# Performance work log

Measured on AMD Instinct MI355X. Metric: run time of the kernel, lower is better.

Reference implementation:

```python
import jax, jax.numpy as jnp
import numpy as np

NEG_INF = -1000000000.0
B, S, E, H = 2, 2048, 1024, 16
HD = E // H


def setup_inputs() -> dict:
    key = jax.random.key(0)
    ks = jax.random.split(key, 5)
    sd = 1.0 / np.sqrt(E)
    return {
        "x": jax.random.normal(ks[0], (B, S, E), dtype=jnp.float32),
        "Wqkv": jax.random.normal(ks[1], (3 * E, E), dtype=jnp.float32) * sd,
        "bqkv": jax.random.normal(ks[2], (3 * E,), dtype=jnp.float32) * sd,
        "Wout": jax.random.normal(ks[3], (E, E), dtype=jnp.float32) * sd,
        "bout": jax.random.normal(ks[4], (E,), dtype=jnp.float32) * sd,
    }


def reference(x, Wqkv, bqkv, Wout, bout):
    # qkv projection (torch Linear: x @ W.T + b)
    qkv = x @ Wqkv.T + bqkv                      # [B, S, 3E]
    qkv = qkv.reshape(B, S, H, 3 * HD).transpose(0, 2, 1, 3)  # [B, H, S, 3*hd]
    q, k, v = jnp.split(qkv, 3, axis=-1)          # each [B, H, S, hd]
    scaled = jnp.einsum('bhqd,bhkd->bhqk', q, k) / jnp.sqrt(jnp.float32(HD))
    # faithful to source: mask = tril(ones) * NEG_INF (lower triangle incl. diagonal gets -1e9)
    mask = jnp.tril(jnp.ones((S, S), dtype=jnp.float32)) * NEG_INF
    scaled = scaled + mask                        # broadcast over [B, H]
    attention = jax.nn.softmax(scaled, axis=-1)
    values = jnp.einsum('bhqk,bhkd->bhqd', attention, v)
    values = values.transpose(0, 2, 1, 3).reshape(B, S, E)
    out = values @ Wout.T + bout
    return out
```

## Files before the change

kernel.cpp:

```cpp
#include <hip/hip_runtime.h>
#include <hip/hip_bf16.h>
#include <math.h>

#define Bb 2
#define Ss 2048
#define Ee 1024
#define Hh 16
#define HDd 64
#define NEG_INF_F -1000000000.0f

typedef __attribute__((ext_vector_type(8))) short bfrag;
typedef __attribute__((ext_vector_type(4))) float ffrag;
typedef __attribute__((ext_vector_type(16))) float ffrag16;
typedef __attribute__((ext_vector_type(8))) unsigned short us8;

#define C1F 0.1803368801f

__device__ __forceinline__ unsigned short f2bf(float x) {
  unsigned u = __float_as_uint(x);
  u += 0x7fffu + ((u >> 16) & 1u);
  return (unsigned short)(u >> 16);
}
__device__ __forceinline__ float bf2f(unsigned short h) {
  return __uint_as_float(((unsigned)h) << 16);
}

__device__ __forceinline__ void async_copy16(void* lds, const void* g) {
  __builtin_amdgcn_global_load_lds(
      (const __attribute__((address_space(1))) unsigned int*)g,
      (__attribute__((address_space(3))) unsigned int*)lds, 16, 0, 0);
}

__global__ __launch_bounds__(256) void split_all(
    const float* __restrict__ x, unsigned short* __restrict__ xh,
    const float* __restrict__ wq, unsigned short* __restrict__ wqh,
    unsigned short* __restrict__ wql,
    const float* __restrict__ wo, unsigned short* __restrict__ woh,
    unsigned short* __restrict__ wol) {
  int bid = blockIdx.x;
  const float* in;
  unsigned short *hi, *lo;
  if (bid < 4096) { in = x; hi = xh; lo = nullptr; }
  else if (bid < 7168) { bid -= 4096; in = wq; hi = wqh; lo = wql; }
  else { bid -= 7168; in = wo; hi = woh; lo = wol; }
  const int idx = (bid * 256 + threadIdx.x) * 4;
  const float4 v = *(const float4*)(in + idx);
  unsigned short h0 = f2bf(v.x), h1 = f2bf(v.y), h2 = f2bf(v.z), h3 = f2bf(v.w);
  ushort4 hv = {h0, h1, h2, h3};
  *(ushort4*)(hi + idx) = hv;
  if (lo) {
    ushort4 lv = {f2bf(v.x - bf2f(h0)), f2bf(v.y - bf2f(h1)),
                  f2bf(v.z - bf2f(h2)), f2bf(v.w - bf2f(h3))};
    *(ushort4*)(lo + idx) = lv;
  }
}

__device__ __forceinline__ int gemm_slot(int row, int q) {
  return (row >> 1) * 8 + ((((row & 1) * 4) | q) ^ ((row >> 1) & 7));
}
__device__ __forceinline__ int slot_src_off(int slot, int ld) {
  const int dr = slot >> 3;
  const int idx8 = (slot & 7) ^ (dr & 7);
  const int row = dr * 2 + (idx8 >> 2);
  const int q = idx8 & 3;
  return row * ld + q * 8;
}

__global__ __launch_bounds__(256) void gemm_qkv(
    const unsigned short* __restrict__ Ah,
    const unsigned short* __restrict__ Bh, const unsigned short* __restrict__ Bl,
    const float* __restrict__ bias,
    unsigned short* __restrict__ q_h,
    unsigned short* __restrict__ k_h, unsigned short* __restrict__ k_l,
    unsigned short* __restrict__ vt_h) {
  __shared__ unsigned short sm[3 * 4096];
  const int tid = threadIdx.x;
  const int lane = tid & 63;
  const int w = tid >> 6;
  const int wm = w >> 1;
  const int wn = w & 1;
  const int l31 = lane & 31;
  const int e = lane >> 5;
  const int m0 = blockIdx.x * 128;
  const int n0 = blockIdx.y * 128;

  int coff[2], ldsb[2];
#pragma unroll
  for (int u = 0; u < 2; ++u) {
    const int slot = w * 128 + u * 64 + lane;
    coff[u] = slot_src_off(slot, 1024);
    ldsb[u] = (w * 128 + u * 64) * 8;
  }
  const unsigned short* srcs[3] = {
      Ah + (size_t)m0 * 1024, Bh + (size_t)n0 * 1024, Bl + (size_t)n0 * 1024};

  ffrag16 acc[2][2];
#pragma unroll
  for (int i = 0; i < 2; ++i)
#pragma unroll
    for (int j = 0; j < 2; ++j) acc[i][j] = (ffrag16)0.f;

  int ca[2][2], cb[2][2];
#pragma unroll
  for (int t = 0; t < 2; ++t)
#pragma unroll
    for (int h2 = 0; h2 < 2; ++h2) {
      ca[t][h2] = gemm_slot(wm * 64 + t * 32 + l31, h2 * 2 + e) * 8;
      cb[t][h2] = gemm_slot(wn * 64 + t * 32 + l31, h2 * 2 + e) * 8;
    }

  for (int k0 = 0; k0 < 1024; k0 += 32) {
    __syncthreads();
#pragma unroll
    for (int t = 0; t < 3; ++t)
#pragma unroll
      for (int u = 0; u < 2; ++u)
        async_copy16(&sm[t * 4096 + ldsb[u]], srcs[t] + coff[u] + k0);
    __syncthreads();

    bfrag ah[2][2], bhf[2][2], blf[2][2];
#pragma unroll
    for (int t = 0; t < 2; ++t)
#pragma unroll
      for (int h2 = 0; h2 < 2; ++h2) {
        ah[t][h2] = *(const bfrag*)&sm[0 * 4096 + ca[t][h2]];
        bhf[t][h2] = *(const bfrag*)&sm[1 * 4096 + cb[t][h2]];
        blf[t][h2] = *(const bfrag*)&sm[2 * 4096 + cb[t][h2]];
      }
#pragma unroll
    for (int mt = 0; mt < 2; ++mt)
#pragma unroll
      for (int nt = 0; nt < 2; ++nt)
#pragma unroll
        for (int h2 = 0; h2 < 2; ++h2) {
          acc[mt][nt] = __builtin_amdgcn_mfma_f32_32x32x16_bf16(
              ah[mt][h2], bhf[nt][h2], acc[mt][nt], 0, 0, 0);
          acc[mt][nt] = __builtin_amdgcn_mfma_f32_32x32x16_bf16(
              ah[mt][h2], blf[nt][h2], acc[mt][nt], 0, 0, 0);
        }
  }

#pragma unroll
  for (int nt = 0; nt < 2; ++nt) {
    const int n = n0 + wn * 64 + nt * 32 + l31;
    const float bv = bias[n];
    const int h = n / 192;
    const int c = n - h * 192;
    const int d = c & 63;
#pragma unroll
    for (int mt = 0; mt < 2; ++mt) {
      if (c >= 128) {
#pragma unroll
        for (int g = 0; g < 4; ++g) {
          const int m = m0 + wm * 64 + mt * 32 + g * 8 + e * 4;
          const int bidx = m >> 11;
          const int s = m & 2047;
          ushort4 hv4;
          unsigned short* ph = (unsigned short*)&hv4;
#pragma unroll
          for (int r = 0; r < 4; ++r)
            ph[r] = f2bf(acc[mt][nt][g * 4 + r] + bv);
          const size_t off =
              (size_t)(bidx * 16 + h) * (64 * 2048) + (size_t)d * 2048 + s;
          *(ushort4*)(vt_h + off) = hv4;
        }
      } else if (c < 64) {
#pragma unroll
        for (int g = 0; g < 4; ++g)
#pragma unroll
          for (int r = 0; r < 4; ++r) {
            const int m = m0 + wm * 64 + mt * 32 + g * 8 + e * 4 + r;
            const int bidx = m >> 11;
            const int s = m & 2047;
            const size_t off =
                (size_t)(bidx * 16 + h) * (2048 * 64) + (size_t)s * 64 + d;
            q_h[off] = f2bf((acc[mt][nt][g * 4 + r] + bv) * C1F);
          }
      } else {
#pragma unroll
        for (int g = 0; g < 4; ++g)
#pragma unroll
          for (int r = 0; r < 4; ++r) {
            const int m = m0 + wm * 64 + mt * 32 + g * 8 + e * 4 + r;
            const int bidx = m >> 11;
            const int s = m & 2047;
            const float val = acc[mt][nt][g * 4 + r] + bv;
            const unsigned short hv = f2bf(val);
            const size_t off =
                (size_t)(bidx * 16 + h) * (2048 * 64) + (size_t)s * 64 + d;
            k_h[off] = hv;
            k_l[off] = f2bf(val - bf2f(hv));
          }
      }
    }
  }
}

__global__ __launch_bounds__(256) void gemm_out2(
    const unsigned short* __restrict__ A,
    const unsigned short* __restrict__ Bh, const unsigned short* __restrict__ Bl,
    const float* __restrict__ bias, float* __restrict__ out) {
  __shared__ unsigned short sm[8192];
  const int tid = threadIdx.x;
  const int lane = tid & 63;
  const int w = tid >> 6;
  const int wm = w >> 1;
  const int wn = w & 1;
  const int l31 = lane & 31;
  const int e = lane >> 5;
  const int m0 = blockIdx.x * 128;
  const int n0 = blockIdx.y * 64;

  int acoff[2], aldsb[2];
#pragma unroll
  for (int u = 0; u < 2; ++u) {
    const int slot = w * 128 + u * 64 + lane;
    acoff[u] = slot_src_off(slot, 1024);
    aldsb[u] = (w * 128 + u * 64) * 8;
  }
  const int bslot = w * 64 + lane;
  const int bcoff = slot_src_off(bslot, 1024);
  const int bldsb = bslot * 8;

  const unsigned short* Ap  = A + (size_t)m0 * 1024;
  const unsigned short* Bph = Bh + (size_t)n0 * 1024;
  const unsigned short* Bpl = Bl + (size_t)n0 * 1024;

  ffrag16 acc[2];
  acc[0] = (ffrag16)0.f;
  acc[1] = (ffrag16)0.f;

  int ca[2][2], cb[2];
#pragma unroll
  for (int t = 0; t < 2; ++t)
#pragma unroll
    for (int h2 = 0; h2 < 2; ++h2)
      ca[t][h2] = gemm_slot(wm * 64 + t * 32 + l31, h2 * 2 + e) * 8;
#pragma unroll
  for (int h2 = 0; h2 < 2; ++h2)
    cb[h2] = gemm_slot(wn * 32 + l31, h2 * 2 + e) * 8;

  for (int k0 = 0; k0 < 1024; k0 += 32) {
    __syncthreads();
#pragma unroll
    for (int u = 0; u < 2; ++u)
      async_copy16(&sm[0 + aldsb[u]], Ap + acoff[u] + k0);
    async_copy16(&sm[4096 + bldsb], Bph + bcoff + k0);
    async_copy16(&sm[6144 + bldsb], Bpl + bcoff + k0);
    __syncthreads();

    bfrag ah[2][2], bhf[2], blf[2];
#pragma unroll
    for (int t = 0; t < 2; ++t)
#pragma unroll
      for (int h2 = 0; h2 < 2; ++h2)
        ah[t][h2] = *(const bfrag*)&sm[0 + ca[t][h2]];
#pragma unroll
    for (int h2 = 0; h2 < 2; ++h2) {
      bhf[h2] = *(const bfrag*)&sm[4096 + cb[h2]];
      blf[h2] = *(const bfrag*)&sm[6144 + cb[h2]];
    }
#pragma unroll
    for (int mt = 0; mt < 2; ++mt)
#pragma unroll
      for (int h2 = 0; h2 < 2; ++h2) {
        acc[mt] = __builtin_amdgcn_mfma_f32_32x32x16_bf16(
            ah[mt][h2], bhf[h2], acc[mt], 0, 0, 0);
        acc[mt] = __builtin_amdgcn_mfma_f32_32x32x16_bf16(
            ah[mt][h2], blf[h2], acc[mt], 0, 0, 0);
      }
  }

  const int n = n0 + wn * 32 + l31;
  const float bv = bias[n];
#pragma unroll
  for (int mt = 0; mt < 2; ++mt)
#pragma unroll
    for (int g = 0; g < 4; ++g)
#pragma unroll
      for (int r = 0; r < 4; ++r) {
        const int m = m0 + wm * 64 + mt * 32 + g * 8 + e * 4 + r;
        out[(size_t)m * 1024 + n] = acc[mt][g * 4 + r] + bv;
      }
}

__global__ __launch_bounds__(256) void attn_pair(
    const unsigned short* __restrict__ qh,
    const unsigned short* __restrict__ kh, const unsigned short* __restrict__ kl,
    const unsigned short* __restrict__ vth,
    unsigned short* __restrict__ vals) {
  __shared__ unsigned short sm[2 * 12288 + 8192];
  const int tid = threadIdx.x;
  const int lane = tid & 63;
  const int w = tid >> 6;
  const int l15 = lane & 15;
  const int quad = lane >> 4;
  const int bh = blockIdx.x;
  const int y = blockIdx.y;
  const int rbase[2] = {64 * y + 16 * w, 64 * (31 - y) + 16 * w};
  const int ktB = 31 - y;
  const bool fix = (y == 0) && (w == 3);
  const size_t base = (size_t)bh * (Ss * HDd);
  const int PB = 24576;

  bfrag Qh[2][2];
#pragma unroll
  for (int mt = 0; mt < 2; ++mt)
#pragma unroll
    for (int ks = 0; ks < 2; ++ks) {
      const size_t off = base + (size_t)(rbase[mt] + l15) * 64 + ks * 32 + quad * 8;
      Qh[mt][ks] = *(const bfrag*)(qh + off);
    }

  bfrag vone;
#pragma unroll
  for (int j = 0; j < 8; ++j) vone[j] = (short)0x3F80;

  const int c0 = w * 128 + lane;
  const int c1 = c0 + 64;
  const int r0 = c0 >> 3, r1 = c1 >> 3;
  const int s0 = ((c0 & 7) ^ (r0 & 7)) * 8;
  const int s1 = ((c1 & 7) ^ (r1 & 7)) * 8;
  const int koff0 = r0 * 64 + s0, koff1 = r1 * 64 + s1;
  const int voff0 = r0 * 2048 + s0, voff1 = r1 * 2048 + s1;
  const int ldsc0 = (w * 128) * 8;
  const int ldsc1 = (w * 128 + 64) * 8;

  ffrag O[2][4], Oe[2], Vsum[4];
#pragma unroll
  for (int mt = 0; mt < 2; ++mt) {
#pragma unroll
    for (int dt = 0; dt < 4; ++dt) O[mt][dt] = (ffrag)0.f;
    Oe[mt] = (ffrag)0.f;
  }
#pragma unroll
  for (int dt = 0; dt < 4; ++dt) Vsum[dt] = (ffrag)0.f;

  {
    const unsigned short* kph = kh + base + y * 4096;
    const unsigned short* kpl = kl + base + y * 4096;
    const unsigned short* vph = vth + base + y * 64;
    async_copy16(&sm[0 + ldsc0], kph + koff0);
    async_copy16(&sm[0 + ldsc1], kph + koff1);
    async_copy16(&sm[4096 + ldsc0], kpl + koff0);
    async_copy16(&sm[4096 + ldsc1], kpl + koff1);
    async_copy16(&sm[8192 + ldsc0], vph + voff0);
    async_copy16(&sm[8192 + ldsc1], vph + voff1);
  }

  int bufo = 0;
  for (int kt = y; kt < 32; ++kt) {
    __syncthreads();
    if (kt + 1 < 32) {
      const int alt = bufo ^ 12288;
      const unsigned short* kph = kh + base + (kt + 1) * 4096;
      const unsigned short* kpl = kl + base + (kt + 1) * 4096;
      const unsigned short* vph = vth + base + (kt + 1) * 64;
      async_copy16(&sm[alt + 0 + ldsc0], kph + koff0);
      async_copy16(&sm[alt + 0 + ldsc1], kph + koff1);
      async_copy16(&sm[alt + 4096 + ldsc0], kpl + koff0);
      async_copy16(&sm[alt + 4096 + ldsc1], kpl + koff1);
      async_copy16(&sm[alt + 8192 + ldsc0], vph + voff0);
      async_copy16(&sm[alt + 8192 + ldsc1], vph + voff1);
    }
    const bool bact = (kt >= ktB);

    ffrag S[2][4];
#pragma unroll
    for (int mt = 0; mt < 2; ++mt)
#pragma unroll
      for (int nt = 0; nt < 4; ++nt) S[mt][nt] = (ffrag)0.f;
#pragma unroll
    for (int nt = 0; nt < 4; ++nt) {
      const int krow = nt * 16 + l15;
#pragma unroll
      for (int ks = 0; ks < 2; ++ks) {
        const int koffr = bufo + krow * 64 + ((ks * 4 + quad) ^ (krow & 7)) * 8;
        const bfrag kbh = *(const bfrag*)&sm[koffr];
        const bfrag kbl = *(const bfrag*)&sm[4096 + koffr];
        S[0][nt] = __builtin_amdgcn_mfma_f32_16x16x32_bf16(Qh[0][ks], kbh, S[0][nt], 0, 0, 0);
        S[0][nt] = __builtin_amdgcn_mfma_f32_16x16x32_bf16(Qh[0][ks], kbl, S[0][nt], 0, 0, 0);
        if (bact) {
          S[1][nt] = __builtin_amdgcn_mfma_f32_16x16x32_bf16(Qh[1][ks], kbh, S[1][nt], 0, 0, 0);
          S[1][nt] = __builtin_amdgcn_mfma_f32_16x16x32_bf16(Qh[1][ks], kbl, S[1][nt], 0, 0, 0);
        }
      }
    }

    const float CM = -1.442695041e9f;
#pragma unroll
    for (int mt = 0; mt < 2; ++mt) {
      if (mt == 1 && !bact) continue;
      const bool partial = (kt == (mt == 0 ? y : ktB));
#pragma unroll
      for (int nt = 0; nt < 4; ++nt) {
        const int key = nt * 16 + l15;
#pragma unroll
        for (int rp = 0; rp < 2; ++rp) {
          float t0 = S[mt][nt][2 * rp];
          float t1 = S[mt][nt][2 * rp + 1];
          if (partial) {
            const int jg = kt * 64 + key;
            const int ig = rbase[mt] + quad * 4 + 2 * rp;
            if (jg <= ig) t0 += CM;
            if (jg <= ig + 1) t1 += CM;
          }
          float2 pf;
          pf.x = __builtin_amdgcn_exp2f(t0);
          pf.y = __builtin_amdgcn_exp2f(t1);
          const __hip_bfloat162 pb = __float22bfloat162_rn(pf);
          const unsigned short* pbs = (const unsigned short*)&pb;
          const int prow0 = w * 32 + mt * 16 + quad * 4 + 2 * rp;
          sm[PB + prow0 * 64 + (((key >> 3) ^ (prow0 & 7)) * 8 + (key & 7))] = pbs[0];
          const int prow1 = prow0 + 1;
          sm[PB + prow1 * 64 + (((key >> 3) ^ (prow1 & 7)) * 8 + (key & 7))] = pbs[1];
        }
      }
    }

#pragma unroll
    for (int ks = 0; ks < 2; ++ks) {
      bfrag pA[2];
#pragma unroll
      for (int mt = 0; mt < 2; ++mt) {
        if (mt == 1 && !bact) continue;
        const int prow = w * 32 + mt * 16 + l15;
        pA[mt] = *(const bfrag*)&sm[PB + prow * 64 + ((ks * 4 + quad) ^ (prow & 7)) * 8];
      }
      Oe[0] = __builtin_amdgcn_mfma_f32_16x16x32_bf16(pA[0], vone, Oe[0], 0, 0, 0);
      if (bact)
        Oe[1] = __builtin_amdgcn_mfma_f32_16x16x32_bf16(pA[1], vone, Oe[1], 0, 0, 0);
#pragma unroll
      for (int dt = 0; dt < 4; ++dt) {
        const int vrow = dt * 16 + l15;
        const int voffr = bufo + 8192 + vrow * 64 + ((ks * 4 + quad) ^ (vrow & 7)) * 8;
        const bfrag vbh = *(const bfrag*)&sm[voffr];
        O[0][dt] = __builtin_amdgcn_mfma_f32_16x16x32_bf16(pA[0], vbh, O[0][dt], 0, 0, 0);
        if (bact)
          O[1][dt] = __builtin_amdgcn_mfma_f32_16x16x32_bf16(pA[1], vbh, O[1][dt], 0, 0, 0);
        if (fix)
          Vsum[dt] = __builtin_amdgcn_mfma_f32_16x16x32_bf16(vone, vbh, Vsum[dt], 0, 0, 0);
      }
    }
    bufo ^= 12288;
  }

  const int b = bh >> 4;
  const int h = bh & 15;
#pragma unroll
  for (int mt = 0; mt < 2; ++mt)
#pragma unroll
    for (int r = 0; r < 4; ++r) {
      const float inv = 1.0f / Oe[mt][r];
      const int s = rbase[mt] + quad * 4 + r;
      const size_t rowoff = ((size_t)b * 2048 + s) * 1024 + h * 64;
#pragma unroll
      for (int dt = 0; dt < 4; ++dt) {
        float val = O[mt][dt][r] * inv;
        if (fix && mt == 1 && quad == 3 && r == 3)
          val = Vsum[dt][r] * (1.0f / 2048.0f);
        vals[rowoff + dt * 16 + l15] = f2bf(val);
      }
    }
}

extern "C" void kernel_launch(void* const* d_in, const int* in_sizes, int n_in,
                              void* d_out, int out_size, void* d_ws, size_t ws_size,
                              hipStream_t stream) {
  const float* x    = (const float*)d_in[0];
  const float* Wqkv = (const float*)d_in[1];
  const float* bqkv = (const float*)d_in[2];
  const float* Wout = (const float*)d_in[3];
  const float* bout = (const float*)d_in[4];
  float* out = (float*)d_out;
  char* wsb = (char*)d_ws;

  unsigned short* qhp  = (unsigned short*)d_ws;
  unsigned short* khp  = qhp + 1 * 4194304;
  unsigned short* klp  = qhp + 2 * 4194304;
  unsigned short* vthp = qhp + 3 * 4194304;
  unsigned short* vals = qhp + 4 * 4194304;
  unsigned short* wqh  = (unsigned short*)(wsb + (48u << 20));
  unsigned short* wql  = (unsigned short*)(wsb + (54u << 20));
  unsigned short* woh  = (unsigned short*)(wsb + (60u << 20));
  unsigned short* wol  = (unsigned short*)(wsb + (62u << 20));
  unsigned short* xh   = (unsigned short*)d_out;

  dim3 blk(256);
  split_all<<<8192, blk, 0, stream>>>(x, xh, Wqkv, wqh, wql, Wout, woh, wol);
  gemm_qkv<<<dim3(32, 24), blk, 0, stream>>>(xh, wqh, wql, bqkv,
                                             qhp, khp, klp, vthp);
  attn_pair<<<dim3(32, 16), blk, 0, stream>>>(qhp, khp, klp, vthp, vals);
  gemm_out2<<<dim3(32, 16), blk, 0, stream>>>(vals, woh, wol, bout, out);
}
```

Measured before the change: 222.2 us.

## Split attention key range across two blocks and merge partial outputs

The attention kernel gains a z dimension that splits each query-pair's key-tile range into two pieces, with a per-row-pair split point chosen to balance work. Each block writes an unnormalised partial output in bf16 plus a row-sum to workspace, and a new merge kernel adds the two partials and normalises into vals. The goal is more blocks and better balance of the uneven causal work. In exchange, LDS double buffering is dropped for a single synchronous buffer with launch bounds asking for 4 blocks per CU, and an extra launch plus a partial-buffer round trip through global memory are added.

```diff
diff --git a/kernel.cpp b/kernel.cpp
--- a/kernel.cpp
+++ b/kernel.cpp
@@ -284,12 +284,12 @@
       }
 }
 
-__global__ __launch_bounds__(256) void attn_pair(
+__global__ __launch_bounds__(256, 4) void attn_ks(
     const unsigned short* __restrict__ qh,
     const unsigned short* __restrict__ kh, const unsigned short* __restrict__ kl,
     const unsigned short* __restrict__ vth,
-    unsigned short* __restrict__ vals) {
-  __shared__ unsigned short sm[2 * 12288 + 8192];
+    unsigned short* __restrict__ pO, float* __restrict__ pl) {
+  __shared__ unsigned short sm[12288 + 8192];
   const int tid = threadIdx.x;
   const int lane = tid & 63;
   const int w = tid >> 6;
@@ -297,11 +297,15 @@
   const int quad = lane >> 4;
   const int bh = blockIdx.x;
   const int y = blockIdx.y;
+  const int z = blockIdx.z;
   const int rbase[2] = {64 * y + 16 * w, 64 * (31 - y) + 16 * w};
   const int ktB = 31 - y;
+  const int E0 = (y <= 7) ? (y + 17) : 24;
+  const int kts = z ? E0 : y;
+  const int kte = z ? 32 : E0;
   const bool fix = (y == 0) && (w == 3);
   const size_t base = (size_t)bh * (Ss * HDd);
-  const int PB = 24576;
+  const int PB = 12288;
 
   bfrag Qh[2][2];
 #pragma unroll
@@ -336,33 +340,19 @@
 #pragma unroll
   for (int dt = 0; dt < 4; ++dt) Vsum[dt] = (ffrag)0.f;
 
-  {
-    const unsigned short* kph = kh + base + y * 4096;
-    const unsigned short* kpl = kl + base + y * 4096;
-    const unsigned short* vph = vth + base + y * 64;
+  for (int kt = kts; kt < kte; ++kt) {
+    const unsigned short* kph = kh + base + kt * 4096;
+    const unsigned short* kpl = kl + base + kt * 4096;
+    const unsigned short* vph = vth + base + kt * 64;
+    __syncthreads();
     async_copy16(&sm[0 + ldsc0], kph + koff0);
     async_copy16(&sm[0 + ldsc1], kph + koff1);
     async_copy16(&sm[4096 + ldsc0], kpl + koff0);
     async_copy16(&sm[4096 + ldsc1], kpl + koff1);
     async_copy16(&sm[8192 + ldsc0], vph + voff0);
     async_copy16(&sm[8192 + ldsc1], vph + voff1);
-  }
-
-  int bufo = 0;
-  for (int kt = y; kt < 32; ++kt) {
     __syncthreads();
-    if (kt + 1 < 32) {
-      const int alt = bufo ^ 12288;
-      const unsigned short* kph = kh + base + (kt + 1) * 4096;
-      const unsigned short* kpl = kl + base + (kt + 1) * 4096;
-      const unsigned short* vph = vth + base + (kt + 1) * 64;
-      async_copy16(&sm[alt + 0 + ldsc0], kph + koff0);
-      async_copy16(&sm[alt + 0 + ldsc1], kph + koff1);
-      async_copy16(&sm[alt + 4096 + ldsc0], kpl + koff0);
-      async_copy16(&sm[alt + 4096 + ldsc1], kpl + koff1);
-      async_copy16(&sm[alt + 8192 + ldsc0], vph + voff0);
-      async_copy16(&sm[alt + 8192 + ldsc1], vph + voff1);
-    }
+
     const bool bact = (kt >= ktB);
 
     ffrag S[2][4];
@@ -375,7 +365,7 @@
       const int krow = nt * 16 + l15;
 #pragma unroll
       for (int ks = 0; ks < 2; ++ks) {
-        const int koffr = bufo + krow * 64 + ((ks * 4 + quad) ^ (krow & 7)) * 8;
+        const int koffr = krow * 64 + ((ks * 4 + quad) ^ (krow & 7)) * 8;
         const bfrag kbh = *(const bfrag*)&sm[koffr];
         const bfrag kbl = *(const bfrag*)&sm[4096 + koffr];
         S[0][nt] = __builtin_amdgcn_mfma_f32_16x16x32_bf16(Qh[0][ks], kbh, S[0][nt], 0, 0, 0);
@@ -433,7 +423,7 @@
 #pragma unroll
       for (int dt = 0; dt < 4; ++dt) {
         const int vrow = dt * 16 + l15;
-        const int voffr = bufo + 8192 + vrow * 64 + ((ks * 4 + quad) ^ (vrow & 7)) * 8;
+        const int voffr = 8192 + vrow * 64 + ((ks * 4 + quad) ^ (vrow & 7)) * 8;
         const bfrag vbh = *(const bfrag*)&sm[voffr];
         O[0][dt] = __builtin_amdgcn_mfma_f32_16x16x32_bf16(pA[0], vbh, O[0][dt], 0, 0, 0);
         if (bact)
@@ -442,26 +432,46 @@
           Vsum[dt] = __builtin_amdgcn_mfma_f32_16x16x32_bf16(vone, vbh, Vsum[dt], 0, 0, 0);
       }
     }
-    bufo ^= 12288;
-  }
-
+  }
+
+  const size_t pbase = (size_t)z * (32 * 2048 * 64) + (size_t)bh * (2048 * 64);
+  const int lbase = z * 65536 + bh * 2048;
+  const float lfix = 64.0f * (float)(kte - kts);
+#pragma unroll
+  for (int mt = 0; mt < 2; ++mt)
+#pragma unroll
+    for (int r = 0; r < 4; ++r) {
+      const int s = rbase[mt] + quad * 4 + r;
+      const bool fl = fix && mt == 1 && quad == 3 && r == 3;
+#pragma unroll
+      for (int dt = 0; dt < 4; ++dt) {
+        const float val = fl ? Vsum[dt][r] : O[mt][dt][r];
+        pO[pbase + (size_t)s * 64 + dt * 16 + l15] = f2bf(val);
+      }
+      if (l15 == 0) pl[lbase + s] = fl ? lfix : Oe[mt][r];
+    }
+}
+
+__global__ __launch_bounds__(256) void merge_vals(
+    const unsigned short* __restrict__ pO, const float* __restrict__ pl,
+    unsigned short* __restrict__ vals) {
+  const int idx = (blockIdx.x * 256 + threadIdx.x) * 4;
+  const int d = idx & 63;
+  const int sbh = idx >> 6;
+  const int s = sbh & 2047;
+  const int bh = sbh >> 11;
+  const size_t zstr = (size_t)32 * 2048 * 64;
+  const ushort4 o0 = *(const ushort4*)(pO + (size_t)sbh * 64 + d);
+  const ushort4 o1 = *(const ushort4*)(pO + zstr + (size_t)sbh * 64 + d);
+  const float inv = 1.0f / (pl[sbh] + pl[65536 + sbh]);
+  ushort4 rv;
+  rv.x = f2bf((bf2f(o0.x) + bf2f(o1.x)) * inv);
+  rv.y = f2bf((bf2f(o0.y) + bf2f(o1.y)) * inv);
+  rv.z = f2bf((bf2f(o0.z) + bf2f(o1.z)) * inv);
+  rv.w = f2bf((bf2f(o0.w) + bf2f(o1.w)) * inv);
   const int b = bh >> 4;
   const int h = bh & 15;
-#pragma unroll
-  for (int mt = 0; mt < 2; ++mt)
-#pragma unroll
-    for (int r = 0; r < 4; ++r) {
-      const float inv = 1.0f / Oe[mt][r];
-      const int s = rbase[mt] + quad * 4 + r;
-      const size_t rowoff = ((size_t)b * 2048 + s) * 1024 + h * 64;
-#pragma unroll
-      for (int dt = 0; dt < 4; ++dt) {
-        float val = O[mt][dt][r] * inv;
-        if (fix && mt == 1 && quad == 3 && r == 3)
-          val = Vsum[dt][r] * (1.0f / 2048.0f);
-        vals[rowoff + dt * 16 + l15] = f2bf(val);
-      }
-    }
+  *(ushort4*)(vals + ((size_t)b * 2048 + s) * 1024 + h * 64 + d) = rv;
 }
 
 extern "C" void kernel_launch(void* const* d_in, const int* in_sizes, int n_in,
@@ -480,6 +490,8 @@
   unsigned short* klp  = qhp + 2 * 4194304;
   unsigned short* vthp = qhp + 3 * 4194304;
   unsigned short* vals = qhp + 4 * 4194304;
+  unsigned short* pO   = (unsigned short*)(wsb + (40u << 20));
+  float*          pl   = (float*)(wsb + (56u << 20));
   unsigned short* wqh  = (unsigned short*)(wsb + (48u << 20));
   unsigned short* wql  = (unsigned short*)(wsb + (54u << 20));
   unsigned short* woh  = (unsigned short*)(wsb + (60u << 20));
@@ -490,6 +502,7 @@
   split_all<<<8192, blk, 0, stream>>>(x, xh, Wqkv, wqh, wql, Wout, woh, wol);
   gemm_qkv<<<dim3(32, 24), blk, 0, stream>>>(xh, wqh, wql, bqkv,
                                              qhp, khp, klp, vthp);
-  attn_pair<<<dim3(32, 16), blk, 0, stream>>>(qhp, khp, klp, vthp, vals);
+  attn_ks<<<dim3(32, 16, 2), blk, 0, stream>>>(qhp, khp, klp, vthp, pO, pl);
+  merge_vals<<<4096, blk, 0, stream>>>(pO, pl, vals);
   gemm_out2<<<dim3(32, 16), blk, 0, stream>>>(vals, woh, wol, bout, out);
 }
```

After: 330.4 us. +48.7%, slower.
